# Kernel tuning notes

Hardware: AMD Instinct MI355X
Metric: run time of the kernel (lower is better)

Reference implementation:

```python
import jax, jax.numpy as jnp
import numpy as np

B, L, D, H = 2, 2048, 1024, 16
DK = D // H


def setup_inputs() -> dict:
    key = jax.random.key(0)
    ks = jax.random.split(key, 11)
    s = 0.02
    return {
        "q": jax.random.normal(ks[0], (B, L, D), jnp.float32),
        "k": jax.random.normal(ks[1], (B, L, D), jnp.float32),
        "v": jax.random.normal(ks[2], (B, L, D), jnp.float32),
        "mask": jnp.ones((B, 1, 1, L), jnp.int32),
        "wq": jax.random.normal(ks[3], (D, D), jnp.float32) * s,
        "bq": jnp.zeros((D,), jnp.float32),
        "wk": jax.random.normal(ks[4], (D, D), jnp.float32) * s,
        "bk": jnp.zeros((D,), jnp.float32),
        "wv": jax.random.normal(ks[5], (D, D), jnp.float32) * s,
        "bv": jnp.zeros((D,), jnp.float32),
        "wo": jax.random.normal(ks[6], (D, D), jnp.float32) * s,
        "bo": jnp.zeros((D,), jnp.float32),
    }


def _split_heads(x):
    # (B, L, D) -> (B, H, L, DK)
    return x.reshape(B, L, H, DK).transpose(0, 2, 1, 3)


def reference(q, k, v, mask, wq, bq, wk, bk, wv, bv, wo, bo):
    query = _split_heads(q @ wq.T + bq)
    key = _split_heads(k @ wk.T + bk)
    value = _split_heads(v @ wv.T + bv)
    scale = 1.0 / jnp.sqrt(jnp.asarray(DK, query.dtype))
    # (B, H, Lq, Lk) materialized scores, as in the original module
    scores = jnp.einsum('bhqd,bhkd->bhqk', query, key) * scale
    scores = jnp.where(mask == 0, jnp.asarray(-1e9, scores.dtype), scores)
    weights = jax.nn.softmax(scores, axis=-1)
    out = jnp.einsum('bhqk,bhkd->bhqd', weights, value)
    out = out.transpose(0, 2, 1, 3).reshape(B, L, D)
    return out @ wo.T + bo
```

## Files before the change

kernel.cpp:

```cpp
#include <hip/hip_runtime.h>
#include <hip/hip_bf16.h>


#define DEVINL __device__ __forceinline__

typedef __attribute__((ext_vector_type(8))) short short8;
typedef __attribute__((ext_vector_type(4))) float floatx4;

static constexpr int Bq = 2, Lq = 2048, Dm = 1024;
static constexpr int Mrows = Bq * Lq;
static constexpr size_t QKV_LD = 3072;

DEVINL unsigned short f2bf(float x) {
  __hip_bfloat16 h = __float2bfloat16(x);
  unsigned short u;
  __builtin_memcpy(&u, &h, 2);
  return u;
}

DEVINL short8 cvt8(float4 a, float4 b) {
  union { unsigned short u[8]; short8 v; } o;
  o.u[0] = f2bf(a.x); o.u[1] = f2bf(a.y); o.u[2] = f2bf(a.z); o.u[3] = f2bf(a.w);
  o.u[4] = f2bf(b.x); o.u[5] = f2bf(b.y); o.u[6] = f2bf(b.z); o.u[7] = f2bf(b.w);
  return o.v;
}

DEVINL void gll16(const void* g, const void* l) {
  auto gp = (const __attribute__((address_space(1))) char*)(unsigned long long)(uintptr_t)g;
  auto lp = (__attribute__((address_space(3))) char*)(unsigned int)(uintptr_t)l;
  __builtin_amdgcn_global_load_lds(gp, lp, 16, 0, 0);
}

template <bool A_BF16, bool OUT_BF16>
__global__ __launch_bounds__(256) void gemm_k(
    const void* __restrict__ A0, const void* __restrict__ A1, const void* __restrict__ A2,
    const float* __restrict__ W0, const float* __restrict__ W1, const float* __restrict__ W2,
    const float* __restrict__ b0, const float* __restrict__ b1, const float* __restrict__ b2,
    void* __restrict__ Cout, int M, int N, int K, int ldc) {
  const int z = blockIdx.z;
  const void* Aany = (z == 0) ? A0 : ((z == 1) ? A1 : A2);
  const float* W = (z == 0) ? W0 : ((z == 1) ? W1 : W2);
  const float* bias = (z == 0) ? b0 : ((z == 1) ? b1 : b2);
  const int m0 = blockIdx.x * 128, n0 = blockIdx.y * 128;
  const int tid = threadIdx.x, lane = tid & 63, w = tid >> 6;
  const int wr = w >> 1, wc = w & 1;

  __shared__ __align__(16) unsigned short As[2][128 * 32];
  __shared__ __align__(16) unsigned short Bs[2][128 * 32];

  floatx4 acc[4][4] = {};
  float4 wreg[2][2], areg[2][2];

  auto loadW = [&](int kt) {
#pragma unroll
    for (int it = 0; it < 2; ++it) {
      int g = it * 256 + tid, row = g >> 2, gk = g & 3;
      const float* p = W + (size_t)(n0 + row) * K + kt + gk * 8;
      wreg[it][0] = ((const float4*)p)[0];
      wreg[it][1] = ((const float4*)p)[1];
    }
  };
  auto loadA = [&](int kt) {
#pragma unroll
    for (int it = 0; it < 2; ++it) {
      int g = it * 256 + tid, row = g >> 2, gk = g & 3;
      const float* p = (const float*)Aany + (size_t)(m0 + row) * K + kt + gk * 8;
      areg[it][0] = ((const float4*)p)[0];
      areg[it][1] = ((const float4*)p)[1];
    }
  };
  auto writeW = [&](int buf) {
#pragma unroll
    for (int it = 0; it < 2; ++it) {
      int g = it * 256 + tid, row = g >> 2, gk = g & 3;
      *(short8*)((char*)Bs + buf * 8192 + row * 64 + ((gk ^ (row & 3)) << 4)) =
          cvt8(wreg[it][0], wreg[it][1]);
    }
  };
  auto writeA = [&](int buf) {
#pragma unroll
    for (int it = 0; it < 2; ++it) {
      int g = it * 256 + tid, row = g >> 2, gk = g & 3;
      *(short8*)((char*)As + buf * 8192 + row * 64 + ((gk ^ (row & 3)) << 4)) =
          cvt8(areg[it][0], areg[it][1]);
    }
  };
  auto stageA = [&](int kt, int buf) {
#pragma unroll
    for (int it = 0; it < 2; ++it) {
      int g = it * 256 + tid, row = g >> 2, gk = g & 3;
      int koff = (gk ^ (row & 3)) * 8;
      gll16((const unsigned short*)Aany + (size_t)(m0 + row) * K + kt + koff,
            (const char*)As + buf * 8192 + (it * 256 + w * 64) * 16);
    }
  };

  const int nt = K / 32;
  loadW(0);
  if (!A_BF16) loadA(0);
  writeW(0);
  if (A_BF16) stageA(0, 0); else writeA(0);
  if (nt > 1) { loadW(32); if (!A_BF16) loadA(32); }
  __syncthreads();

  const int krow = lane >> 4;
  for (int t = 0; t < nt; ++t) {
    const int c = t & 1, n = c ^ 1;
    if (t + 1 < nt) {
      writeW(n);
      if (A_BF16) stageA((t + 1) * 32, n); else writeA(n);
      if (t + 2 < nt) { loadW((t + 2) * 32); if (!A_BF16) loadA((t + 2) * 32); }
    }
    short8 af[4], bf[4];
#pragma unroll
    for (int m = 0; m < 4; ++m) {
      int row = wr * 64 + m * 16 + (lane & 15);
      af[m] = *(const short8*)((const char*)As + c * 8192 + row * 64 + ((krow ^ (row & 3)) << 4));
    }
#pragma unroll
    for (int n2 = 0; n2 < 4; ++n2) {
      int row = wc * 64 + n2 * 16 + (lane & 15);
      bf[n2] = *(const short8*)((const char*)Bs + c * 8192 + row * 64 + ((krow ^ (row & 3)) << 4));
    }
    __builtin_amdgcn_s_setprio(1);
#pragma unroll
    for (int m = 0; m < 4; ++m)
#pragma unroll
      for (int n2 = 0; n2 < 4; ++n2)
        acc[m][n2] = __builtin_amdgcn_mfma_f32_16x16x32_bf16(af[m], bf[n2], acc[m][n2], 0, 0, 0);
    __builtin_amdgcn_s_setprio(0);
    __syncthreads();
  }

  const int r4 = lane >> 4;
#pragma unroll
  for (int m = 0; m < 4; ++m)
#pragma unroll
    for (int n2 = 0; n2 < 4; ++n2) {
      int col = n0 + wc * 64 + n2 * 16 + (lane & 15);
      float bv = bias[col];
#pragma unroll
      for (int r = 0; r < 4; ++r) {
        int row = m0 + wr * 64 + m * 16 + r4 * 4 + r;
        float v = acc[m][n2][r] + bv;
        if (OUT_BF16)
          ((unsigned short*)Cout)[(size_t)row * ldc + (size_t)z * N + col] = f2bf(v);
        else
          ((float*)Cout)[(size_t)row * ldc + (size_t)z * N + col] = v;
      }
    }
}

__global__ __launch_bounds__(256) void attn_kernel(const unsigned short* __restrict__ QKV,
                                                   const int* __restrict__ mask,
                                                   unsigned short* __restrict__ Aout) {
  const int bh = blockIdx.y, b = bh >> 4, h = bh & 15;
  const int q0 = blockIdx.x * 64;
  const int tid = threadIdx.x, lane = tid & 63, w = tid >> 6;

  __shared__ __align__(16) unsigned short Klds[2][64 * 64];
  __shared__ __align__(16) unsigned short Vtlds[2][64 * 64];
  __shared__ __align__(16) unsigned short Plds[4][16 * 64];

  const unsigned short* base = QKV + (size_t)b * Lq * QKV_LD;
  const unsigned short* Kbase = base + 1024;
  const unsigned short* Vbase = base + 2048;

  short8 qf[2];
  {
    int row = q0 + w * 16 + (lane & 15);
#pragma unroll
    for (int c = 0; c < 2; ++c)
      qf[c] = *(const short8*)(base + (size_t)row * QKV_LD + h * 64 + c * 32 + (lane >> 4) * 8);
  }

  const int kp = tid & 31;
  const int vd0 = (tid >> 5) * 8;

  auto stageK = [&](int t, int buf) {
#pragma unroll
    for (int it = 0; it < 2; ++it) {
      int g = it * 256 + tid, key = g >> 3, gk = g & 7;
      gll16(Kbase + (size_t)(t * 64 + key) * QKV_LD + h * 64 + (gk ^ (key & 7)) * 8,
            (const char*)Klds + buf * 8192 + (it * 256 + w * 64) * 16);
    }
  };
  short8 vr0, vr1;
  auto loadV = [&](int t) {
    vr0 = *(const short8*)(Vbase + (size_t)(t * 64 + 2 * kp) * QKV_LD + h * 64 + vd0);
    vr1 = *(const short8*)(Vbase + (size_t)(t * 64 + 2 * kp + 1) * QKV_LD + h * 64 + vd0);
  };
  auto writeV = [&](int buf) {
#pragma unroll
    for (int i = 0; i < 8; ++i) {
      int d = vd0 + i;
      unsigned int val = (unsigned int)(unsigned short)vr0[i] |
                         ((unsigned int)(unsigned short)vr1[i] << 16);
      *(unsigned int*)((char*)Vtlds + buf * 8192 + d * 128 + (((kp >> 2) ^ (d & 7)) << 4) +
                       (kp & 3) * 4) = val;
    }
  };

  stageK(0, 0);
  loadV(0);
  writeV(0);
  __syncthreads();

  floatx4 o[4] = {};
  float mrow[4], lrow[4];
#pragma unroll
  for (int r = 0; r < 4; ++r) { mrow[r] = -1e30f; lrow[r] = 0.f; }

  for (int t = 0; t < Lq / 64; ++t) {
    const int c = t & 1, n = c ^ 1;
    if (t + 1 < Lq / 64) { stageK(t + 1, n); loadV(t + 1); }

    floatx4 s[4] = {};
    __builtin_amdgcn_s_setprio(1);
#pragma unroll
    for (int f = 0; f < 4; ++f) {
      int key = f * 16 + (lane & 15);
#pragma unroll
      for (int c2 = 0; c2 < 2; ++c2) {
        short8 kf = *(const short8*)((const char*)Klds + c * 8192 + key * 128 +
                                     (((c2 * 4 + (lane >> 4)) ^ (key & 7)) << 4));
        s[f] = __builtin_amdgcn_mfma_f32_16x16x32_bf16(qf[c2], kf, s[f], 0, 0, 0);
      }
    }
    __builtin_amdgcn_s_setprio(0);

    float tmax[4] = {-1e30f, -1e30f, -1e30f, -1e30f};
#pragma unroll
    for (int f = 0; f < 4; ++f) {
      int mv = mask[b * Lq + t * 64 + f * 16 + (lane & 15)];
#pragma unroll
      for (int r = 0; r < 4; ++r) {
        float sv = s[f][r] * 0.125f;
        sv = mv ? sv : -1e9f;
        s[f][r] = sv;
        tmax[r] = fmaxf(tmax[r], sv);
      }
    }
#pragma unroll
    for (int dx = 1; dx <= 8; dx <<= 1)
#pragma unroll
      for (int r = 0; r < 4; ++r) tmax[r] = fmaxf(tmax[r], __shfl_xor(tmax[r], dx, 64));

    float mnew[4], alpha[4], rsum[4] = {0, 0, 0, 0};
#pragma unroll
    for (int r = 0; r < 4; ++r) {
      mnew[r] = fmaxf(mrow[r], tmax[r]);
      alpha[r] = __expf(mrow[r] - mnew[r]);
      mrow[r] = mnew[r];
    }
#pragma unroll
    for (int f = 0; f < 4; ++f)
#pragma unroll
      for (int r = 0; r < 4; ++r) {
        float p = __expf(s[f][r] - mnew[r]);
        s[f][r] = p;
        rsum[r] += p;
      }
#pragma unroll
    for (int dx = 1; dx <= 8; dx <<= 1)
#pragma unroll
      for (int r = 0; r < 4; ++r) rsum[r] += __shfl_xor(rsum[r], dx, 64);
#pragma unroll
    for (int r = 0; r < 4; ++r) lrow[r] = lrow[r] * alpha[r] + rsum[r];
#pragma unroll
    for (int df = 0; df < 4; ++df)
#pragma unroll
      for (int r = 0; r < 4; ++r) o[df][r] *= alpha[r];

#pragma unroll
    for (int f = 0; f < 4; ++f)
#pragma unroll
      for (int r = 0; r < 4; ++r) {
        int row = (lane >> 4) * 4 + r, col = f * 16 + (lane & 15);
        *(unsigned short*)((char*)&Plds[w][0] + row * 128 + (((col >> 3) ^ (row & 7)) << 4) +
                           (col & 7) * 2) = f2bf(s[f][r]);
      }

    short8 pf[2];
#pragma unroll
    for (int kc = 0; kc < 2; ++kc)
      pf[kc] = *(const short8*)((const char*)&Plds[w][0] + (lane & 15) * 128 +
                                (((kc * 4 + (lane >> 4)) ^ (lane & 7)) << 4));
    __builtin_amdgcn_s_setprio(1);
#pragma unroll
    for (int df = 0; df < 4; ++df) {
      int d = df * 16 + (lane & 15);
#pragma unroll
      for (int kc = 0; kc < 2; ++kc) {
        short8 vf = *(const short8*)((const char*)Vtlds + c * 8192 + d * 128 +
                                     (((kc * 4 + (lane >> 4)) ^ (d & 7)) << 4));
        o[df] = __builtin_amdgcn_mfma_f32_16x16x32_bf16(pf[kc], vf, o[df], 0, 0, 0);
      }
    }
    __builtin_amdgcn_s_setprio(0);

    if (t + 1 < Lq / 64) writeV(n);
    __syncthreads();
  }

#pragma unroll
  for (int df = 0; df < 4; ++df)
#pragma unroll
    for (int r = 0; r < 4; ++r) {
      int row = q0 + w * 16 + (lane >> 4) * 4 + r;
      int col = h * 64 + df * 16 + (lane & 15);
      Aout[(size_t)(b * Lq + row) * Dm + col] = f2bf(o[df][r] / lrow[r]);
    }
}

extern "C" void kernel_launch(void* const* d_in, const int* in_sizes, int n_in,
                              void* d_out, int out_size, void* d_ws, size_t ws_size,
                              hipStream_t stream) {
  const float* q = (const float*)d_in[0];
  const float* k = (const float*)d_in[1];
  const float* v = (const float*)d_in[2];
  const int* maskp = (const int*)d_in[3];
  const float* wq = (const float*)d_in[4];
  const float* bq = (const float*)d_in[5];
  const float* wk = (const float*)d_in[6];
  const float* bk = (const float*)d_in[7];
  const float* wv = (const float*)d_in[8];
  const float* bv = (const float*)d_in[9];
  const float* wo = (const float*)d_in[10];
  const float* bo = (const float*)d_in[11];

  unsigned short* qkv = (unsigned short*)d_ws;
  unsigned short* attnout = qkv + (size_t)Mrows * QKV_LD;

  gemm_k<false, true><<<dim3(Mrows / 128, Dm / 128, 3), 256, 0, stream>>>(
      q, k, v, wq, wk, wv, bq, bk, bv, qkv, Mrows, Dm, Dm, (int)QKV_LD);

  attn_kernel<<<dim3(Lq / 64, Bq * 16), 256, 0, stream>>>(qkv, maskp, attnout);

  gemm_k<true, false><<<dim3(Mrows / 128, Dm / 128, 1), 256, 0, stream>>>(
      attnout, attnout, attnout, wo, wo, wo, bo, bo, bo, d_out, Mrows, Dm, Dm, Dm);
}
```

Before: 316.1 us.

## Add lazy softmax rescaling, precomputed mask flags, MFMA row sums, and reordered GEMM loads

The attention kernel now folds the 1/8 scale into Q once. It precomputes a per-tile all-ones mask flag in shared memory. It skips the max shuffle and rescale when the new tile max stays within a threshold of the running max. The row-sum shuffle reduction is replaced by an MFMA against a ones vector, using the bf16 P values. The GEMM loop issues LDS fragment reads and MFMAs before the next-tile staging writes, so the compute overlaps the prefetch. These changes aim to cut VALU and cross-lane shuffle work in softmax, at the cost of extra MFMAs, slightly different rounding (Q scaled in bf16, sums taken from bf16 P), and branch divergence.

```diff
diff --git a/kernel.cpp b/kernel.cpp
--- a/kernel.cpp
+++ b/kernel.cpp
@@ -10,12 +10,20 @@
 static constexpr int Bq = 2, Lq = 2048, Dm = 1024;
 static constexpr int Mrows = Bq * Lq;
 static constexpr size_t QKV_LD = 3072;
+static constexpr int NT = Lq / 64;
 
 DEVINL unsigned short f2bf(float x) {
   __hip_bfloat16 h = __float2bfloat16(x);
   unsigned short u;
   __builtin_memcpy(&u, &h, 2);
   return u;
+}
+
+DEVINL float bf2f(unsigned short u) {
+  unsigned int t = ((unsigned int)u) << 16;
+  float f;
+  __builtin_memcpy(&f, &t, 4);
+  return f;
 }
 
 DEVINL short8 cvt8(float4 a, float4 b) {
@@ -106,29 +114,29 @@
   const int krow = lane >> 4;
   for (int t = 0; t < nt; ++t) {
     const int c = t & 1, n = c ^ 1;
+    short8 af[4], bfr[4];
+#pragma unroll
+    for (int m = 0; m < 4; ++m) {
+      int row = wr * 64 + m * 16 + (lane & 15);
+      af[m] = *(const short8*)((const char*)As + c * 8192 + row * 64 + ((krow ^ (row & 3)) << 4));
+    }
+#pragma unroll
+    for (int n2 = 0; n2 < 4; ++n2) {
+      int row = wc * 64 + n2 * 16 + (lane & 15);
+      bfr[n2] = *(const short8*)((const char*)Bs + c * 8192 + row * 64 + ((krow ^ (row & 3)) << 4));
+    }
+    __builtin_amdgcn_s_setprio(1);
+#pragma unroll
+    for (int m = 0; m < 4; ++m)
+#pragma unroll
+      for (int n2 = 0; n2 < 4; ++n2)
+        acc[m][n2] = __builtin_amdgcn_mfma_f32_16x16x32_bf16(af[m], bfr[n2], acc[m][n2], 0, 0, 0);
+    __builtin_amdgcn_s_setprio(0);
     if (t + 1 < nt) {
       writeW(n);
       if (A_BF16) stageA((t + 1) * 32, n); else writeA(n);
       if (t + 2 < nt) { loadW((t + 2) * 32); if (!A_BF16) loadA((t + 2) * 32); }
     }
-    short8 af[4], bf[4];
-#pragma unroll
-    for (int m = 0; m < 4; ++m) {
-      int row = wr * 64 + m * 16 + (lane & 15);
-      af[m] = *(const short8*)((const char*)As + c * 8192 + row * 64 + ((krow ^ (row & 3)) << 4));
-    }
-#pragma unroll
-    for (int n2 = 0; n2 < 4; ++n2) {
-      int row = wc * 64 + n2 * 16 + (lane & 15);
-      bf[n2] = *(const short8*)((const char*)Bs + c * 8192 + row * 64 + ((krow ^ (row & 3)) << 4));
-    }
-    __builtin_amdgcn_s_setprio(1);
-#pragma unroll
-    for (int m = 0; m < 4; ++m)
-#pragma unroll
-      for (int n2 = 0; n2 < 4; ++n2)
-        acc[m][n2] = __builtin_amdgcn_mfma_f32_16x16x32_bf16(af[m], bf[n2], acc[m][n2], 0, 0, 0);
-    __builtin_amdgcn_s_setprio(0);
     __syncthreads();
   }
 
@@ -161,18 +169,11 @@
   __shared__ __align__(16) unsigned short Klds[2][64 * 64];
   __shared__ __align__(16) unsigned short Vtlds[2][64 * 64];
   __shared__ __align__(16) unsigned short Plds[4][16 * 64];
+  __shared__ int mflag[NT];
 
   const unsigned short* base = QKV + (size_t)b * Lq * QKV_LD;
   const unsigned short* Kbase = base + 1024;
   const unsigned short* Vbase = base + 2048;
-
-  short8 qf[2];
-  {
-    int row = q0 + w * 16 + (lane & 15);
-#pragma unroll
-    for (int c = 0; c < 2; ++c)
-      qf[c] = *(const short8*)(base + (size_t)row * QKV_LD + h * 64 + c * 32 + (lane >> 4) * 8);
-  }
 
   const int kp = tid & 31;
   const int vd0 = (tid >> 5) * 8;
@@ -204,16 +205,42 @@
   stageK(0, 0);
   loadV(0);
   writeV(0);
+  {
+    const int* mp = mask + b * Lq + tid * 8;
+    int4 a = ((const int4*)mp)[0], bb = ((const int4*)mp)[1];
+    int myall = (a.x && a.y && a.z && a.w && bb.x && bb.y && bb.z && bb.w) ? 1 : 0;
+    unsigned long long bal = __ballot(myall);
+    if (lane < 8) mflag[w * 8 + lane] = (((bal >> (lane * 8)) & 0xffull) == 0xffull);
+  }
+
+  short8 qf[2];
+  {
+    int row = q0 + w * 16 + (lane & 15);
+#pragma unroll
+    for (int c = 0; c < 2; ++c) {
+      short8 raw = *(const short8*)(base + (size_t)row * QKV_LD + h * 64 + c * 32 + (lane >> 4) * 8);
+      union { unsigned short u[8]; short8 v; } o2;
+#pragma unroll
+      for (int i = 0; i < 8; ++i) o2.u[i] = f2bf(bf2f((unsigned short)raw[i]) * 0.125f);
+      qf[c] = o2.v;
+    }
+  }
+  union { unsigned short u[8]; short8 v; } one_u;
+#pragma unroll
+  for (int i = 0; i < 8; ++i) one_u.u[i] = 0x3F80;
+  const short8 ones8 = one_u.v;
+
   __syncthreads();
 
   floatx4 o[4] = {};
-  float mrow[4], lrow[4];
-#pragma unroll
-  for (int r = 0; r < 4; ++r) { mrow[r] = -1e30f; lrow[r] = 0.f; }
-
-  for (int t = 0; t < Lq / 64; ++t) {
+  floatx4 lacc = {};
+  float mrow[4];
+#pragma unroll
+  for (int r = 0; r < 4; ++r) mrow[r] = -1e30f;
+
+  for (int t = 0; t < NT; ++t) {
     const int c = t & 1, n = c ^ 1;
-    if (t + 1 < Lq / 64) { stageK(t + 1, n); loadV(t + 1); }
+    if (t + 1 < NT) { stageK(t + 1, n); loadV(t + 1); }
 
     floatx4 s[4] = {};
     __builtin_amdgcn_s_setprio(1);
@@ -229,48 +256,51 @@
     }
     __builtin_amdgcn_s_setprio(0);
 
-    float tmax[4] = {-1e30f, -1e30f, -1e30f, -1e30f};
-#pragma unroll
-    for (int f = 0; f < 4; ++f) {
-      int mv = mask[b * Lq + t * 64 + f * 16 + (lane & 15)];
+    float tmax[4];
+#pragma unroll
+    for (int r = 0; r < 4; ++r)
+      tmax[r] = fmaxf(fmaxf(s[0][r], s[1][r]), fmaxf(s[2][r], s[3][r]));
+    const int allm = mflag[t];
+    bool ok = (tmax[0] <= mrow[0] + 8.f) && (tmax[1] <= mrow[1] + 8.f) &&
+              (tmax[2] <= mrow[2] + 8.f) && (tmax[3] <= mrow[3] + 8.f);
+    if (__ballot(ok && allm) == ~0ull) {
+#pragma unroll
+      for (int f = 0; f < 4; ++f)
+#pragma unroll
+        for (int r = 0; r < 4; ++r) s[f][r] = __expf(s[f][r] - mrow[r]);
+    } else {
+#pragma unroll
+      for (int dx = 1; dx <= 8; dx <<= 1)
+#pragma unroll
+        for (int r = 0; r < 4; ++r) tmax[r] = fmaxf(tmax[r], __shfl_xor(tmax[r], dx, 64));
+      float mnew[4], alpha[4];
 #pragma unroll
       for (int r = 0; r < 4; ++r) {
-        float sv = s[f][r] * 0.125f;
-        sv = mv ? sv : -1e9f;
-        s[f][r] = sv;
-        tmax[r] = fmaxf(tmax[r], sv);
-      }
-    }
-#pragma unroll
-    for (int dx = 1; dx <= 8; dx <<= 1)
-#pragma unroll
-      for (int r = 0; r < 4; ++r) tmax[r] = fmaxf(tmax[r], __shfl_xor(tmax[r], dx, 64));
-
-    float mnew[4], alpha[4], rsum[4] = {0, 0, 0, 0};
-#pragma unroll
-    for (int r = 0; r < 4; ++r) {
-      mnew[r] = fmaxf(mrow[r], tmax[r]);
-      alpha[r] = __expf(mrow[r] - mnew[r]);
-      mrow[r] = mnew[r];
-    }
-#pragma unroll
-    for (int f = 0; f < 4; ++f)
-#pragma unroll
-      for (int r = 0; r < 4; ++r) {
-        float p = __expf(s[f][r] - mnew[r]);
-        s[f][r] = p;
-        rsum[r] += p;
-      }
-#pragma unroll
-    for (int dx = 1; dx <= 8; dx <<= 1)
-#pragma unroll
-      for (int r = 0; r < 4; ++r) rsum[r] += __shfl_xor(rsum[r], dx, 64);
-#pragma unroll
-    for (int r = 0; r < 4; ++r) lrow[r] = lrow[r] * alpha[r] + rsum[r];
-#pragma unroll
-    for (int df = 0; df < 4; ++df)
-#pragma unroll
-      for (int r = 0; r < 4; ++r) o[df][r] *= alpha[r];
+        mnew[r] = fmaxf(mrow[r], tmax[r]);
+        alpha[r] = __expf(mrow[r] - mnew[r]);
+        mrow[r] = mnew[r];
+      }
+#pragma unroll
+      for (int df = 0; df < 4; ++df)
+#pragma unroll
+        for (int r = 0; r < 4; ++r) o[df][r] *= alpha[r];
+#pragma unroll
+      for (int r = 0; r < 4; ++r) lacc[r] *= alpha[r];
+      if (allm) {
+#pragma unroll
+        for (int f = 0; f < 4; ++f)
+#pragma unroll
+          for (int r = 0; r < 4; ++r) s[f][r] = __expf(s[f][r] - mnew[r]);
+      } else {
+#pragma unroll
+        for (int f = 0; f < 4; ++f) {
+          int mv = mask[b * Lq + t * 64 + f * 16 + (lane & 15)];
+#pragma unroll
+          for (int r = 0; r < 4; ++r)
+            s[f][r] = mv ? __expf(s[f][r] - mnew[r]) : 0.f;
+        }
+      }
+    }
 
 #pragma unroll
     for (int f = 0; f < 4; ++f)
@@ -287,6 +317,8 @@
       pf[kc] = *(const short8*)((const char*)&Plds[w][0] + (lane & 15) * 128 +
                                 (((kc * 4 + (lane >> 4)) ^ (lane & 7)) << 4));
     __builtin_amdgcn_s_setprio(1);
+    lacc = __builtin_amdgcn_mfma_f32_16x16x32_bf16(pf[0], ones8, lacc, 0, 0, 0);
+    lacc = __builtin_amdgcn_mfma_f32_16x16x32_bf16(pf[1], ones8, lacc, 0, 0, 0);
 #pragma unroll
     for (int df = 0; df < 4; ++df) {
       int d = df * 16 + (lane & 15);
@@ -299,17 +331,20 @@
     }
     __builtin_amdgcn_s_setprio(0);
 
-    if (t + 1 < Lq / 64) writeV(n);
+    if (t + 1 < NT) writeV(n);
     __syncthreads();
   }
 
+  float rl[4];
+#pragma unroll
+  for (int r = 0; r < 4; ++r) rl[r] = 1.0f / lacc[r];
 #pragma unroll
   for (int df = 0; df < 4; ++df)
 #pragma unroll
     for (int r = 0; r < 4; ++r) {
       int row = q0 + w * 16 + (lane >> 4) * 4 + r;
       int col = h * 64 + df * 16 + (lane & 15);
-      Aout[(size_t)(b * Lq + row) * Dm + col] = f2bf(o[df][r] / lrow[r]);
+      Aout[(size_t)(b * Lq + row) * Dm + col] = f2bf(o[df][r] * rl[r]);
     }
 }
 
```

Result: faster. 276.3 us (-12.6%).
